# Kernel tuning notes

Hardware: AMD Instinct MI355X
Metric: run time of the kernel (lower is better)

## Reference

```python
import jax, jax.numpy as jnp
import numpy as np

C = 66  # channels (joints)
NB_CLASSES = 14
T = 96


def conv1d(x, w, b, pad, groups=1):
    # x: (N, Cin, L), w: (Cout, Cin//groups, K)
    y = jax.lax.conv_general_dilated(
        x, w, window_strides=(1,), padding=[(pad, pad)],
        feature_group_count=groups, dimension_numbers=('NCH', 'OIH', 'NCH'))
    return y + b[None, :, None]


def pool2(x):
    # AvgPool1d(kernel_size=2) along last axis
    return x.reshape(*x.shape[:-1], x.shape[-1] // 2, 2).mean(-1)


def setup_inputs() -> dict:
    key = jax.random.key(0)
    ks = jax.random.split(key, 16)

    def xavier(k, shape, fan_in, fan_out, gain=jnp.sqrt(2.0)):
        bound = gain * jnp.sqrt(6.0 / (fan_in + fan_out))
        return jax.random.uniform(k, shape, jnp.float32, -bound, bound)

    B = 2048
    x = jax.random.normal(ks[0], (B, T, C), jnp.float32)
    # shared convs (same weights for every channel)
    w_hs = xavier(ks[1], (8, 1, 7), 1 * 7, 8 * 7)
    b_hs = jnp.full((8,), 0.1, jnp.float32)
    w_ls = xavier(ks[2], (8, 1, 3), 1 * 3, 8 * 3)
    b_ls = jnp.full((8,), 0.1, jnp.float32)
    # per-channel individual convs, packed for grouped conv (groups=C)
    w_hi1 = xavier(ks[3], (C * 4, 8, 7), 8 * 7, 4 * 7)
    b_hi1 = jnp.full((C * 4,), 0.1, jnp.float32)
    w_hi2 = xavier(ks[4], (C * 4, 4, 7), 4 * 7, 4 * 7)
    b_hi2 = jnp.full((C * 4,), 0.1, jnp.float32)
    w_li1 = xavier(ks[5], (C * 4, 8, 3), 8 * 3, 4 * 3)
    b_li1 = jnp.full((C * 4,), 0.1, jnp.float32)
    w_li2 = xavier(ks[6], (C * 4, 4, 3), 4 * 3, 4 * 3)
    b_li2 = jnp.full((C * 4,), 0.1, jnp.float32)
    # MLP
    F_IN = 9 * C * 12
    w_fc1 = xavier(ks[7], (1936, F_IN), F_IN, 1936)
    b_fc1 = jnp.full((1936,), 0.1, jnp.float32)
    w_fc2 = xavier(ks[8], (NB_CLASSES, 1936), 1936, NB_CLASSES)
    b_fc2 = jnp.full((NB_CLASSES,), 0.1, jnp.float32)
    return dict(x=x, w_hs=w_hs, b_hs=b_hs, w_ls=w_ls, b_ls=b_ls,
                w_hi1=w_hi1, b_hi1=b_hi1, w_hi2=w_hi2, b_hi2=b_hi2,
                w_li1=w_li1, b_li1=b_li1, w_li2=w_li2, b_li2=b_li2,
                w_fc1=w_fc1, b_fc1=b_fc1, w_fc2=w_fc2, b_fc2=b_fc2)


def _branch(xc_flat, B, w_s, b_s, w_i1, b_i1, w_i2, b_i2, pad):
    # xc_flat: (B*C, 1, T). Shared conv applied per channel, then grouped
    # (per-channel) convs with groups=C.
    h = pool2(jax.nn.relu(conv1d(xc_flat, w_s, b_s, pad)))       # (B*C, 8, 48)
    h = h.reshape(B, C * 8, T // 2)
    h = pool2(jax.nn.relu(conv1d(h, w_i1, b_i1, pad, groups=C)))  # (B, C*4, 24)
    h = pool2(jax.nn.relu(conv1d(h, w_i2, b_i2, pad, groups=C)))  # (B, C*4, 12)
    return h.reshape(B, C, 4, T // 8)


def reference(x, w_hs, b_hs, w_ls, b_ls, w_hi1, b_hi1, w_hi2, b_hi2,
              w_li1, b_li1, w_li2, b_li2, w_fc1, b_fc1, w_fc2, b_fc2):
    B = x.shape[0]
    xc = jnp.transpose(x, (0, 2, 1))            # (B, C, T)
    xc_flat = xc.reshape(B * C, 1, T)
    high = _branch(xc_flat, B, w_hs, b_hs, w_hi1, b_hi1, w_hi2, b_hi2, pad=3)
    low = _branch(xc_flat, B, w_ls, b_ls, w_li1, b_li1, w_li2, b_li2, pad=1)
    orig = pool2(pool2(pool2(xc)))[:, :, None, :]  # (B, C, 1, 12)
    # per-channel concat order: [original, low, high] -> (B, C, 9, 12)
    feat = jnp.concatenate([orig, low, high], axis=2).reshape(B, 9 * C * 12)
    h = jax.nn.relu(feat @ w_fc1.T + b_fc1)
    return h @ w_fc2.T + b_fc2
```

## Files before the change

kernel.cpp:

```cpp
#include <hip/hip_runtime.h>
#include <hip/hip_bf16.h>

#define T_LEN 96
#define C_CH  66
#define FIN   7128
#define KPAD  7168
#define NFC1  1936
#define NPAD  2048
#define NCLS  14

typedef __bf16 bf16x8 __attribute__((ext_vector_type(8)));
typedef float  f32x4  __attribute__((ext_vector_type(4)));

#define GLD_LDS(gp, lp) __builtin_amdgcn_global_load_lds(                     \
    (__attribute__((address_space(1))) void*)(gp),                            \
    (__attribute__((address_space(3))) void*)(lp), 16, 0, 0)

__global__ __launch_bounds__(256) void transpose_kernel(
    const float* __restrict__ x, float* __restrict__ xT, int B)
{
    __shared__ float tile[64][65];
    const int t = threadIdx.x & 63;
    const int w = threadIdx.x >> 6;
    const int tc0 = blockIdx.x * 64;
    const int b0  = blockIdx.y * 64;
    #pragma unroll
    for (int j = 0; j < 16; j++) {
        const int r = w * 16 + j;
        tile[r][t] = x[(size_t)(b0 + r) * (T_LEN * C_CH) + tc0 + t];
    }
    __syncthreads();
    #pragma unroll
    for (int j = 0; j < 16; j++) {
        const int r = w * 16 + j;
        xT[(size_t)(tc0 + r) * B + b0 + t] = tile[t][r];
    }
}

__global__ __launch_bounds__(256) void pad_w_kernel(
    const float* __restrict__ w, __hip_bfloat16* __restrict__ wb)
{
    int idx = blockIdx.x * 256 + threadIdx.x;
    int row = idx / 896;
    int cc  = idx - row * 896;
    float4 a = {0.f, 0.f, 0.f, 0.f}, b = {0.f, 0.f, 0.f, 0.f};
    if (row < NFC1 && cc < 891) {
        const float4* src = (const float4*)(w + (size_t)row * FIN + cc * 8);
        a = src[0];
        b = src[1];
    }
    __align__(16) __hip_bfloat16 v[8];
    v[0] = __float2bfloat16(a.x); v[1] = __float2bfloat16(a.y);
    v[2] = __float2bfloat16(a.z); v[3] = __float2bfloat16(a.w);
    v[4] = __float2bfloat16(b.x); v[5] = __float2bfloat16(b.y);
    v[6] = __float2bfloat16(b.z); v[7] = __float2bfloat16(b.w);
    *(int4*)(wb + (size_t)row * KPAD + cc * 8) = *(const int4*)v;
}

template <int K, bool DO_EXTRA>
__device__ __forceinline__ void conv_branch(
    const float* __restrict__ xb, int ts,
    const float* __restrict__ wS, const float* __restrict__ bS,
    const float* __restrict__ wi1, const float* __restrict__ bi1,
    const float* __restrict__ wi2, const float* __restrict__ bi2,
    __hip_bfloat16* __restrict__ frow, int out_off)
{
    constexpr int PAD = K / 2;
    constexpr int XW  = 24 + 6 * PAD;
    constexpr int THW = 12 + 2 * PAD;

    float s2phR[4][24];

    #pragma unroll
    for (int tt = 0; tt < 4; tt++) {
        float xw[XW];
        #pragma unroll
        for (int i = 0; i < XW; i++) {
            const int t = 24 * tt - 3 * PAD + i;
            xw[i] = (t >= 0 && t < T_LEN) ? xb[(size_t)t * ts] : 0.f;
        }

        if (DO_EXTRA) {
            #pragma unroll
            for (int r = 0; r < 3; r++) {
                float s = 0.f;
                #pragma unroll
                for (int k = 0; k < 8; k++) s += xw[3 * PAD + 8 * r + k];
                frow[3 * tt + r] = __float2bfloat16(s * 0.125f);
            }
        }

        float s2a[4][12];
        #pragma unroll
        for (int oc = 0; oc < 4; oc++) {
            const float bv = bi1[oc];
            #pragma unroll
            for (int q = 0; q < 12; q++) s2a[oc][q] = bv;
        }

        #pragma unroll 1
        for (int ic = 0; ic < 8; ic++) {
            const float bs1 = bS[ic];
            float thw[THW];
            #pragma unroll
            for (int j = 0; j < THW; j++) {
                const int jg = 12 * tt - PAD + j;
                if (jg < 0 || jg >= 48) { thw[j] = 0.f; continue; }
                float y0 = bs1, y1 = bs1;
                #pragma unroll
                for (int k = 0; k < K; k++) {
                    const float w = wS[ic * K + k];
                    y0 = fmaf(w, xw[2 * j + k], y0);
                    y1 = fmaf(w, xw[2 * j + 1 + k], y1);
                }
                thw[j] = 0.5f * (fmaxf(y0, 0.f) + fmaxf(y1, 0.f));
            }
            #pragma unroll
            for (int q = 0; q < 12; q++) {
                #pragma unroll
                for (int oc = 0; oc < 4; oc++) {
                    float a = s2a[oc][q];
                    #pragma unroll
                    for (int k = 0; k < K; k++)
                        a = fmaf(wi1[(oc * 8 + ic) * K + k], thw[q + k], a);
                    s2a[oc][q] = a;
                }
            }
        }

        #pragma unroll
        for (int oc = 0; oc < 4; oc++)
            #pragma unroll
            for (int r = 0; r < 6; r++)
                s2phR[oc][6 * tt + r] =
                    0.5f * (fmaxf(s2a[oc][2 * r], 0.f) +
                            fmaxf(s2a[oc][2 * r + 1], 0.f));
    }

    #pragma unroll 1
    for (int oc = 0; oc < 4; oc++) {
        const float bv = bi2[oc];
        #pragma unroll
        for (int q = 0; q < 12; q++) {
            float y0 = bv, y1 = bv;
            #pragma unroll
            for (int ic = 0; ic < 4; ic++) {
                #pragma unroll
                for (int k = 0; k < K; k++) {
                    const float w = wi2[(oc * 4 + ic) * K + k];
                    const int i0 = 2 * q + k - PAD;
                    const int i1 = 2 * q + 1 + k - PAD;
                    if (i0 >= 0 && i0 < 24) y0 = fmaf(w, s2phR[ic][i0], y0);
                    if (i1 >= 0 && i1 < 24) y1 = fmaf(w, s2phR[ic][i1], y1);
                }
            }
            frow[out_off + oc * 12 + q] =
                __float2bfloat16(0.5f * (fmaxf(y0, 0.f) + fmaxf(y1, 0.f)));
        }
    }
}

__global__ __launch_bounds__(64, 2) void conv_fused_kernel(
    const float* __restrict__ x, int ts, int bs, int cs,
    const float* __restrict__ w_hs, const float* __restrict__ b_hs,
    const float* __restrict__ w_ls, const float* __restrict__ b_ls,
    const float* __restrict__ w_hi1, const float* __restrict__ b_hi1,
    const float* __restrict__ w_hi2, const float* __restrict__ b_hi2,
    const float* __restrict__ w_li1, const float* __restrict__ b_li1,
    const float* __restrict__ w_li2, const float* __restrict__ b_li2,
    __hip_bfloat16* __restrict__ feat)
{
    const int lane = threadIdx.x;
    const int b = blockIdx.x * 64 + lane;
    const int c = blockIdx.y;
    const float* xb = x + (size_t)b * bs + (size_t)c * cs;
    __hip_bfloat16* frow = feat + (size_t)b * KPAD + c * 108;

    if (blockIdx.z == 0) {
        conv_branch<7, false>(xb, ts, w_hs, b_hs,
                              w_hi1 + c * 224, b_hi1 + c * 4,
                              w_hi2 + c * 112, b_hi2 + c * 4, frow, 60);
    } else {
        if (c == 0) {
            int4* tail = (int4*)(feat + (size_t)b * KPAD + FIN);
            const int4 z = {0, 0, 0, 0};
            #pragma unroll
            for (int i = 0; i < 5; i++) tail[i] = z;
        }
        conv_branch<3, true>(xb, ts, w_ls, b_ls,
                             w_li1 + c * 96, b_li1 + c * 4,
                             w_li2 + c * 48, b_li2 + c * 4, frow, 12);
    }
}

__global__ __launch_bounds__(256) void gemm_kernel(
    const __hip_bfloat16* __restrict__ A,
    const __hip_bfloat16* __restrict__ Bw,
    float* __restrict__ Cm, int kchunk)
{
    __shared__ __align__(16) __hip_bfloat16 As[4096];
    __shared__ __align__(16) __hip_bfloat16 Bs[4096];

    const int tid  = threadIdx.x;
    const int lane = tid & 63;
    const int wid  = tid >> 6;
    const int m0 = blockIdx.y * 128;
    const int n0 = blockIdx.x * 128;
    const int wm = (wid >> 1) * 64;
    const int wn = (wid & 1) * 64;
    const int lr = lane & 15;
    const int quad = lane >> 4;

    const int r0 = tid >> 2, c0 = (tid & 3) * 8;
    const __hip_bfloat16* gA0 = A  + (size_t)(m0 + r0) * KPAD + c0;
    const __hip_bfloat16* gA1 = gA0 + (size_t)64 * KPAD;
    const __hip_bfloat16* gB0 = Bw + (size_t)(n0 + r0) * KPAD + c0;
    const __hip_bfloat16* gB1 = gB0 + (size_t)64 * KPAD;
    __hip_bfloat16* lA0 = As + wid * 512;
    __hip_bfloat16* lA1 = As + 2048 + wid * 512;
    __hip_bfloat16* lB0 = Bs + wid * 512;
    __hip_bfloat16* lB1 = Bs + 2048 + wid * 512;

    f32x4 acc[4][4] = {};

    const int kBeg = blockIdx.z * kchunk;
    const int kEnd = kBeg + kchunk;
    for (int k0 = kBeg; k0 < kEnd; k0 += 32) {
        __syncthreads();
        GLD_LDS(gA0 + k0, lA0);
        GLD_LDS(gA1 + k0, lA1);
        GLD_LDS(gB0 + k0, lB0);
        GLD_LDS(gB1 + k0, lB1);
        __syncthreads();
        bf16x8 af[4], bfr[4];
        #pragma unroll
        for (int mt = 0; mt < 4; mt++)
            af[mt] = *(const bf16x8*)(As + (wm + mt * 16 + lr) * 32 + quad * 8);
        #pragma unroll
        for (int nt = 0; nt < 4; nt++)
            bfr[nt] = *(const bf16x8*)(Bs + (wn + nt * 16 + lr) * 32 + quad * 8);
        #pragma unroll
        for (int mt = 0; mt < 4; mt++)
            #pragma unroll
            for (int nt = 0; nt < 4; nt++)
                acc[mt][nt] = __builtin_amdgcn_mfma_f32_16x16x32_bf16(
                    af[mt], bfr[nt], acc[mt][nt], 0, 0, 0);
    }

    float* Cs = Cm + (size_t)blockIdx.z * NPAD * NPAD;
    #pragma unroll
    for (int mt = 0; mt < 4; mt++) {
        #pragma unroll
        for (int nt = 0; nt < 4; nt++) {
            const int col = n0 + wn + nt * 16 + lr;
            const int rb  = m0 + wm + mt * 16 + quad * 4;
            #pragma unroll
            for (int r = 0; r < 4; r++)
                Cs[(size_t)(rb + r) * NPAD + col] = acc[mt][nt][r];
        }
    }
}

__global__ __launch_bounds__(256) void fc2_kernel(
    const float* __restrict__ h1, const float* __restrict__ b1,
    const float* __restrict__ w2, const float* __restrict__ b2,
    float* __restrict__ out, int nslab)
{
    const int b = blockIdx.x;
    const int tid = threadIdx.x;
    float acc[NCLS];
    #pragma unroll
    for (int o = 0; o < NCLS; o++) acc[o] = 0.f;
    for (int n = tid; n < NFC1; n += 256) {
        float hv = b1[n];
        for (int s = 0; s < nslab; s++)
            hv += h1[(size_t)s * NPAD * NPAD + (size_t)b * NPAD + n];
        float h = fmaxf(hv, 0.f);
        #pragma unroll
        for (int o = 0; o < NCLS; o++)
            acc[o] = fmaf(h, w2[o * NFC1 + n], acc[o]);
    }
    __shared__ float red[4][NCLS];
    #pragma unroll
    for (int o = 0; o < NCLS; o++) {
        float v = acc[o];
        #pragma unroll
        for (int s = 32; s > 0; s >>= 1) v += __shfl_down(v, s);
        if ((tid & 63) == 0) red[tid >> 6][o] = v;
    }
    __syncthreads();
    if (tid < NCLS)
        out[b * NCLS + tid] = red[0][tid] + red[1][tid] + red[2][tid] +
                              red[3][tid] + b2[tid];
}

extern "C" void kernel_launch(void* const* d_in, const int* in_sizes, int n_in,
                              void* d_out, int out_size, void* d_ws, size_t ws_size,
                              hipStream_t stream)
{
    (void)n_in; (void)out_size;
    const float* x     = (const float*)d_in[0];
    const float* w_hs  = (const float*)d_in[1];
    const float* b_hs  = (const float*)d_in[2];
    const float* w_ls  = (const float*)d_in[3];
    const float* b_ls  = (const float*)d_in[4];
    const float* w_hi1 = (const float*)d_in[5];
    const float* b_hi1 = (const float*)d_in[6];
    const float* w_hi2 = (const float*)d_in[7];
    const float* b_hi2 = (const float*)d_in[8];
    const float* w_li1 = (const float*)d_in[9];
    const float* b_li1 = (const float*)d_in[10];
    const float* w_li2 = (const float*)d_in[11];
    const float* b_li2 = (const float*)d_in[12];
    const float* w_fc1 = (const float*)d_in[13];
    const float* b_fc1 = (const float*)d_in[14];
    const float* w_fc2 = (const float*)d_in[15];
    const float* b_fc2 = (const float*)d_in[16];
    float* out = (float*)d_out;

    const int B = in_sizes[0] / (T_LEN * C_CH);

    char* ws = (char*)d_ws;
    const size_t featB = (size_t)B * KPAD * 2;
    const size_t wbB   = (size_t)NPAD * KPAD * 2;
    const size_t slabB = (size_t)NPAD * NPAD * 4;
    const size_t xtB   = (size_t)T_LEN * C_CH * B * 4;
    const size_t base2 = featB + wbB;

    __hip_bfloat16* feat = (__hip_bfloat16*)ws;
    __hip_bfloat16* wb   = (__hip_bfloat16*)(ws + featB);
    float* h1            = (float*)(ws + base2);

    const int sk = (ws_size >= base2 + 4 * slabB) ? 4 : 2;
    const bool use_xt = (ws_size >= base2 + sk * slabB + xtB);
    float* xT = (float*)(ws + base2 + sk * slabB);

    pad_w_kernel<<<dim3((NPAD * 896) / 256), 256, 0, stream>>>(w_fc1, wb);

    const float* cx = x;
    int ts = C_CH, bsi = T_LEN * C_CH, cs = 1;
    if (use_xt) {
        transpose_kernel<<<dim3(99, B / 64), 256, 0, stream>>>(x, xT, B);
        cx = xT; ts = C_CH * B; bsi = 1; cs = B;
    }
    conv_fused_kernel<<<dim3(B / 64, C_CH, 2), 64, 0, stream>>>(
        cx, ts, bsi, cs, w_hs, b_hs, w_ls, b_ls,
        w_hi1, b_hi1, w_hi2, b_hi2, w_li1, b_li1, w_li2, b_li2, feat);
    gemm_kernel<<<dim3(NPAD / 128, B / 128, sk), 256, 0, stream>>>(
        feat, wb, h1, KPAD / sk);
    fc2_kernel<<<dim3(B), 256, 0, stream>>>(h1, b_fc1, w_fc2, b_fc2, out, sk);
}
```

Baseline: 426.2 us.

## Stream conv stages in finer time chunks with rolling register buffer

```diff
diff --git a/kernel.cpp b/kernel.cpp
--- a/kernel.cpp
+++ b/kernel.cpp
@@ -66,36 +66,41 @@
     __hip_bfloat16* __restrict__ frow, int out_off)
 {
     constexpr int PAD = K / 2;
-    constexpr int XW  = 24 + 6 * PAD;
-    constexpr int THW = 12 + 2 * PAD;
-
-    float s2phR[4][24];
-
-    #pragma unroll
-    for (int tt = 0; tt < 4; tt++) {
-        float xw[XW];
-        #pragma unroll
-        for (int i = 0; i < XW; i++) {
-            const int t = 24 * tt - 3 * PAD + i;
+    constexpr int THW = 6 + 2 * PAD;
+    constexpr int XW  = 12 + 6 * PAD;
+    constexpr int XWL = DO_EXTRA ? (XW + 2) : XW;
+
+    float rg[4][12];
+
+    #pragma unroll
+    for (int tt = 0; tt < 8; tt++) {
+        const int X0 = 12 * tt - 3 * PAD;
+        float xw[XWL];
+        #pragma unroll
+        for (int i = 0; i < XWL; i++) {
+            const int t = X0 + i;
             xw[i] = (t >= 0 && t < T_LEN) ? xb[(size_t)t * ts] : 0.f;
         }
 
         if (DO_EXTRA) {
             #pragma unroll
-            for (int r = 0; r < 3; r++) {
-                float s = 0.f;
-                #pragma unroll
-                for (int k = 0; k < 8; k++) s += xw[3 * PAD + 8 * r + k];
-                frow[3 * tt + r] = __float2bfloat16(s * 0.125f);
+            for (int r = 0; r < 12; r++) {
+                const int lo = 8 * r - X0;
+                if (lo >= 0 && lo + 8 <= XWL) {
+                    float s = 0.f;
+                    #pragma unroll
+                    for (int k = 0; k < 8; k++) s += xw[lo + k];
+                    frow[r] = __float2bfloat16(s * 0.125f);
+                }
             }
         }
 
-        float s2a[4][12];
+        float s2a[4][6];
         #pragma unroll
         for (int oc = 0; oc < 4; oc++) {
             const float bv = bi1[oc];
             #pragma unroll
-            for (int q = 0; q < 12; q++) s2a[oc][q] = bv;
+            for (int q = 0; q < 6; q++) s2a[oc][q] = bv;
         }
 
         #pragma unroll 1
@@ -104,8 +109,8 @@
             float thw[THW];
             #pragma unroll
             for (int j = 0; j < THW; j++) {
-                const int jg = 12 * tt - PAD + j;
-                if (jg < 0 || jg >= 48) { thw[j] = 0.f; continue; }
+                const int p = 6 * tt - PAD + j;
+                if (p < 0 || p >= 48) { thw[j] = 0.f; continue; }
                 float y0 = bs1, y1 = bs1;
                 #pragma unroll
                 for (int k = 0; k < K; k++) {
@@ -116,7 +121,7 @@
                 thw[j] = 0.5f * (fmaxf(y0, 0.f) + fmaxf(y1, 0.f));
             }
             #pragma unroll
-            for (int q = 0; q < 12; q++) {
+            for (int q = 0; q < 6; q++) {
                 #pragma unroll
                 for (int oc = 0; oc < 4; oc++) {
                     float a = s2a[oc][q];
@@ -131,36 +136,42 @@
         #pragma unroll
         for (int oc = 0; oc < 4; oc++)
             #pragma unroll
-            for (int r = 0; r < 6; r++)
-                s2phR[oc][6 * tt + r] =
+            for (int r = 0; r < 3; r++)
+                rg[oc][(3 * tt + r) % 12] =
                     0.5f * (fmaxf(s2a[oc][2 * r], 0.f) +
                             fmaxf(s2a[oc][2 * r + 1], 0.f));
-    }
-
-    #pragma unroll 1
-    for (int oc = 0; oc < 4; oc++) {
-        const float bv = bi2[oc];
+
         #pragma unroll
         for (int q = 0; q < 12; q++) {
-            float y0 = bv, y1 = bv;
-            #pragma unroll
-            for (int ic = 0; ic < 4; ic++) {
+            const bool now    = (2 * q + PAD + 1 <= 3 * tt + 2) || (tt == 7);
+            const bool before = (tt > 0) && (2 * q + PAD + 1 <= 3 * tt - 1);
+            if (now && !before) {
                 #pragma unroll
-                for (int k = 0; k < K; k++) {
-                    const float w = wi2[(oc * 4 + ic) * K + k];
-                    const int i0 = 2 * q + k - PAD;
-                    const int i1 = 2 * q + 1 + k - PAD;
-                    if (i0 >= 0 && i0 < 24) y0 = fmaf(w, s2phR[ic][i0], y0);
-                    if (i1 >= 0 && i1 < 24) y1 = fmaf(w, s2phR[ic][i1], y1);
+                for (int oc = 0; oc < 4; oc++) {
+                    float y0 = bi2[oc], y1 = bi2[oc];
+                    #pragma unroll
+                    for (int ic = 0; ic < 4; ic++) {
+                        #pragma unroll
+                        for (int k = 0; k < K; k++) {
+                            const float w = wi2[(oc * 4 + ic) * K + k];
+                            const int i0 = 2 * q + k - PAD;
+                            const int i1 = i0 + 1;
+                            if (i0 >= 0 && i0 < 24)
+                                y0 = fmaf(w, rg[ic][i0 % 12], y0);
+                            if (i1 >= 0 && i1 < 24)
+                                y1 = fmaf(w, rg[ic][i1 % 12], y1);
+                        }
+                    }
+                    frow[out_off + oc * 12 + q] =
+                        __float2bfloat16(0.5f * (fmaxf(y0, 0.f) +
+                                                 fmaxf(y1, 0.f)));
                 }
             }
-            frow[out_off + oc * 12 + q] =
-                __float2bfloat16(0.5f * (fmaxf(y0, 0.f) + fmaxf(y1, 0.f)));
-        }
-    }
-}
-
-__global__ __launch_bounds__(64, 2) void conv_fused_kernel(
+        }
+    }
+}
+
+__global__ __launch_bounds__(256, 3) void conv_fused_kernel(
     const float* __restrict__ x, int ts, int bs, int cs,
     const float* __restrict__ w_hs, const float* __restrict__ b_hs,
     const float* __restrict__ w_ls, const float* __restrict__ b_ls,
@@ -170,13 +181,14 @@
     const float* __restrict__ w_li2, const float* __restrict__ b_li2,
     __hip_bfloat16* __restrict__ feat)
 {
-    const int lane = threadIdx.x;
-    const int b = blockIdx.x * 64 + lane;
+    const int lane = threadIdx.x & 63;
+    const int wsub = threadIdx.x >> 6;
+    const int b = blockIdx.z * 256 + wsub * 64 + lane;
     const int c = blockIdx.y;
     const float* xb = x + (size_t)b * bs + (size_t)c * cs;
     __hip_bfloat16* frow = feat + (size_t)b * KPAD + c * 108;
 
-    if (blockIdx.z == 0) {
+    if (blockIdx.x == 0) {
         conv_branch<7, false>(xb, ts, w_hs, b_hs,
                               w_hi1 + c * 224, b_hi1 + c * 4,
                               w_hi2 + c * 112, b_hi2 + c * 4, frow, 60);
@@ -343,7 +355,7 @@
         transpose_kernel<<<dim3(99, B / 64), 256, 0, stream>>>(x, xT, B);
         cx = xT; ts = C_CH * B; bsi = 1; cs = B;
     }
-    conv_fused_kernel<<<dim3(B / 64, C_CH, 2), 64, 0, stream>>>(
+    conv_fused_kernel<<<dim3(2, C_CH, B / 256), 256, 0, stream>>>(
         cx, ts, bsi, cs, w_hs, b_hs, w_ls, b_ls,
         w_hi1, b_hi1, w_hi2, b_hi2, w_li1, b_li1, w_li2, b_li2, feat);
     gemm_kernel<<<dim3(NPAD / 128, B / 128, sk), 256, 0, stream>>>(
```

Result: slower. 487.1 us (+14.3%).
